# Optimization experiments

Measured on AMD Instinct MI355X. Metric: run time of the kernel, lower is better.

Reference implementation:

```python
import jax, jax.numpy as jnp
import numpy as np

H = 16   # num_heads
G = 4    # groups (code structurally requires 4)
DIM = 1024
HD = DIM // H // G  # 16


def setup_inputs() -> dict:
    key = jax.random.key(0)
    k1, k2, k3 = jax.random.split(key, 3)
    x = jax.random.normal(k1, (8, 4096, DIM), dtype=jnp.float32)
    w_qkvw = jax.random.normal(k2, (DIM, 4 * DIM), dtype=jnp.float32) * 0.02
    w_out = jax.random.normal(k3, (DIM, DIM), dtype=jnp.float32) * 0.02
    return {"x": x, "w_qkvw": w_qkvw, "w_out": w_out}


def reference(x, w_qkvw, w_out):
    B, S, dim = x.shape
    qkvw = x @ w_qkvw  # [B, S, 4*dim]
    # chunk into G groups along last dim -> G tensors of [B, S, dim] (G==4)
    chunks = jnp.split(qkvw, G, axis=-1)
    # each chunk split again into G sub-chunks of [B, S, dim/G]
    subs = [jnp.split(t, G, axis=-1) for t in chunks]
    # torch: q,k,v,w = [cat([qi,ki,vi,wi], dim=0) for qi,ki,vi,wi in zip(*subs)]
    q = jnp.concatenate([subs[i][0] for i in range(4)], axis=0)  # [4B, S, dim/G]
    k = jnp.concatenate([subs[i][1] for i in range(4)], axis=0)
    v = jnp.concatenate([subs[i][2] for i in range(4)], axis=0)
    w = jnp.concatenate([subs[i][3] for i in range(4)], axis=0)
    # faithful row-major reshape: [4B, S, dim/G] -> [4B, H, S, hd] -> transpose(1,2)
    def shp(t):
        return t.reshape(B * G, H, -1, HD).swapaxes(1, 2)  # [4B, S, H, hd]
    q, k, v = shp(q), shp(k), shp(v)
    w = w.reshape(B * G, H, -1, HD)  # [4B, H, S, hd]
    scale = HD ** -0.5
    scores = (q @ k.swapaxes(-2, -1)) * scale          # [4B, S, H, H]
    attn = jax.nn.softmax(scores, axis=-1)
    o = (attn @ v).swapaxes(1, 2).reshape(B, S, dim)   # [B, S, dim]
    return (o * w.reshape(B, S, dim)) @ w_out
```

## Files before the change

kernel.cpp:

```cpp
#include <hip/hip_runtime.h>
#include <hip/hip_bf16.h>
#include <stdint.h>


typedef __bf16 bf16;
typedef __bf16 bf16x8 __attribute__((ext_vector_type(8)));
typedef float f32x4 __attribute__((ext_vector_type(4)));

__device__ __forceinline__ void gload16(const bf16* g, bf16* l) {
  __builtin_amdgcn_global_load_lds(
      (const __attribute__((address_space(1))) void*)g,
      (__attribute__((address_space(3))) void*)l, 16, 0, 0);
}

#define BAR() asm volatile("s_barrier" ::: "memory")
#define SB() __builtin_amdgcn_sched_barrier(0)
#define LGKM0 asm volatile("s_waitcnt lgkmcnt(0)" ::: "memory")
#define PRIO1 __builtin_amdgcn_s_setprio(1)
#define PRIO0 __builtin_amdgcn_s_setprio(0)

#define READ_A(mq, AO)                                                        \
  {                                                                           \
    _Pragma("unroll") for (int i = 0; i < 4; ++i)                             \
        _Pragma("unroll") for (int kk = 0; kk < 2; ++kk)                      \
            a[i][kk] = *(const bf16x8*)(lds + (AO) +                          \
                                        ((mq)*64 + i * 16 + fr) * 128 +       \
                                        ((kk * 64 + fkb) ^ xo));              \
  }
#define READ_B(nh, BO)                                                        \
  {                                                                           \
    _Pragma("unroll") for (int j = 0; j < 2; ++j)                             \
        _Pragma("unroll") for (int kk = 0; kk < 2; ++kk)                      \
            b[(nh)*2 + j][kk] = *(const bf16x8*)(lds + (BO) +                 \
                                                 (bro + (nh)*32 + j * 16 + fr) * 128 + \
                                                 ((kk * 64 + fkb) ^ xo));     \
  }
#define MFMA_Q(mq, nh)                                                        \
  {                                                                           \
    _Pragma("unroll") for (int i = 0; i < 4; ++i)                             \
        _Pragma("unroll") for (int j = 0; j < 2; ++j) {                       \
      acc[(mq)*4 + i][(nh)*2 + j] = __builtin_amdgcn_mfma_f32_16x16x32_bf16(  \
          a[i][0], b[(nh)*2 + j][0], acc[(mq)*4 + i][(nh)*2 + j], 0, 0, 0);   \
      acc[(mq)*4 + i][(nh)*2 + j] = __builtin_amdgcn_mfma_f32_16x16x32_bf16(  \
          a[i][1], b[(nh)*2 + j][1], acc[(mq)*4 + i][(nh)*2 + j], 0, 0, 0);   \
    }                                                                         \
  }
#define STAGE_AH(h, X, base)                                                  \
  {                                                                           \
    const bf16* g = gA + ((h)*128) * 1024 + (X)*64;                           \
    gload16(g, (bf16*)(lds + (base) + (h)*16384 + wv * 1024));                \
    gload16(g + 64 * 1024, (bf16*)(lds + (base) + (h)*16384 + 8192 + wv * 1024)); \
  }
#define STAGE_BH(h, X)                                                        \
  {                                                                           \
    const int ro = 98304 + ((X)&1) * 32768 + (h)*16384;                       \
    const bf16* g = gB + ((h)*128) * 1024 + (X)*64;                           \
    gload16(g, (bf16*)(lds + ro + wv * 1024));                                \
    gload16(g + 64 * 1024, (bf16*)(lds + ro + 8192 + wv * 1024));             \
  }

template <typename OutT>
__global__ __launch_bounds__(512, 2)
void gemm256(const bf16* __restrict__ A, const bf16* __restrict__ BT,
             OutT* __restrict__ C, int N, int super) {
  constexpr int K = 1024;
  __shared__ __align__(16) char smem[163840];
  char* lds = smem;

  const int tid = threadIdx.x;
  const int lane = tid & 63;
  const int wv = tid >> 6;
  const int wr = wv >> 2;
  const int wc = wv & 3;

  const int gx = gridDim.x;
  const int nwg = gx * gridDim.y;
  const int bid = blockIdx.y * gx + blockIdx.x;
  const int xcd = bid & 7;
  const int l = bid >> 3;
  long trow, tcol;
  if (super) {
    const int s = l >> 5, i = l & 31;
    const int colS = gx >> 2;
    trow = xcd * 16 + (s / colS) * 8 + (i >> 2);
    tcol = (s % colS) * 4 + (i & 3);
  } else {
    const int swz = xcd * (nwg >> 3) + l;
    trow = swz / gx;
    tcol = swz % gx;
  }
  const long row0 = trow * 256;
  const long col0 = tcol * 256;

  const int srow = tid >> 3;
  const int scol = (((tid & 7) * 16) ^ ((srow & 7) << 4)) >> 1;
  const bf16* gA = A + (row0 + srow) * K + scol;
  const bf16* gB = BT + (col0 + srow) * K + scol;

  const int fr = lane & 15;
  const int fkb = (lane >> 4) * 16;
  const int xo = (fr & 7) << 4;
  const int bro = (wc & 1) * 64;

  bf16x8 a[4][2], b[4][2];
  f32x4 acc[8][4] = {};

  STAGE_AH(0, 0, 0); STAGE_AH(1, 0, 0);
  STAGE_AH(0, 1, 32768); STAGE_AH(1, 1, 32768);
  STAGE_BH(0, 0); STAGE_BH(1, 0);
  STAGE_BH(0, 1); STAGE_BH(1, 1);
  asm volatile("s_waitcnt vmcnt(4)" ::: "memory");
  SB(); BAR(); SB();
  READ_A(0, wr * 16384);
  READ_B(0, 98304 + (wc >> 1) * 16384);
  SB();

  int ac0 = 0, ac1 = 32768, ac2 = 65536;
  for (int T = 0; T < 16; ++T) {
    const int aoff = ac0 + wr * 16384;
    const int aoffN = ac1 + wr * 16384;
    const int boff = 98304 + (T & 1) * 32768 + (wc >> 1) * 16384;
    const int boffN = 98304 + ((T + 1) & 1) * 32768 + (wc >> 1) * 16384;
    if (T < 14) { STAGE_AH(0, T + 2, ac2); STAGE_AH(1, T + 2, ac2); }
    SB(); BAR(); LGKM0; SB();
    READ_B(1, boff); SB();
    PRIO1; MFMA_Q(0, 0); PRIO0; SB();
    BAR(); LGKM0; SB();
    PRIO1; MFMA_Q(0, 1); PRIO0; SB();
    READ_A(1, aoff); SB();
    BAR(); LGKM0; SB();
    PRIO1; MFMA_Q(1, 1); PRIO0; SB();
    if (T < 14) {
      STAGE_BH(0, T + 2); STAGE_BH(1, T + 2);
      asm volatile("s_waitcnt vmcnt(8)" ::: "memory");
    } else if (T == 14) {
      asm volatile("s_waitcnt vmcnt(0)" ::: "memory");
    }
    SB(); BAR(); LGKM0; SB();
    PRIO1; MFMA_Q(1, 0); PRIO0; SB();
    if (T < 15) { READ_A(0, aoffN); READ_B(0, boffN); }
    SB();
    const int t = ac0; ac0 = ac1; ac1 = ac2; ac2 = t;
  }

  const int crow = (lane >> 4) * 4;
  const int ccol = lane & 15;
  const long rb = row0 + wr * 128;
  const long cb = col0 + wc * 64;
#pragma unroll
  for (int m = 0; m < 8; ++m)
#pragma unroll
    for (int n = 0; n < 4; ++n)
#pragma unroll
      for (int i = 0; i < 4; ++i)
        C[(rb + m * 16 + crow + i) * (long)N + cb + n * 16 + ccol] =
            (OutT)acc[m][n][i];
}

__device__ __forceinline__ void load16f(const bf16* p, float* f) {
  const uint4* u = (const uint4*)p;
  uint4 a = u[0], b = u[1];
  uint32_t w[8] = {a.x, a.y, a.z, a.w, b.x, b.y, b.z, b.w};
#pragma unroll
  for (int j = 0; j < 8; ++j) {
    f[2 * j] = __uint_as_float(w[j] << 16);
    f[2 * j + 1] = __uint_as_float(w[j] & 0xffff0000u);
  }
}

__global__ __launch_bounds__(256)
void attn_fuse(const bf16* __restrict__ qkvw, bf16* __restrict__ ow,
               int b0, long bstride) {
  __shared__ bf16 data[16 * 1024];
  const int s_hi = blockIdx.x;
  const int g = blockIdx.y;
  const int bz = blockIdx.z;
  const int b = b0 + bz;
  const bf16* base = qkvw + (long)bz * bstride;
  const int tid = threadIdx.x;

#pragma unroll
  for (int i = 0; i < 8; ++i) {
    int c = tid + i * 256;
    int h = c >> 7;
    int col = (c & 127) * 8;
    *(uint4*)&data[h * 1024 + col] =
        *(const uint4*)(base + (long)(h * 256 + s_hi) * 4096 + g * 1024 + col);
  }
  __syncthreads();

  const int s_lo = tid >> 4;
  const int h1 = tid & 15;
  const int off = s_lo * 16;

  float q[16], p[16], o[16];
  load16f(&data[h1 * 1024 + off], q);

  float mx = -1e30f;
#pragma unroll
  for (int h2 = 0; h2 < 16; ++h2) {
    float kf[16];
    load16f(&data[h2 * 1024 + 256 + off], kf);
    float s = 0.f;
#pragma unroll
    for (int d = 0; d < 16; ++d) s += q[d] * kf[d];
    s *= 0.25f;
    p[h2] = s;
    mx = fmaxf(mx, s);
  }
  float sum = 0.f;
#pragma unroll
  for (int h2 = 0; h2 < 16; ++h2) {
    float e = __expf(p[h2] - mx);
    p[h2] = e;
    sum += e;
  }
  const float inv = 1.f / sum;
#pragma unroll
  for (int d = 0; d < 16; ++d) o[d] = 0.f;
#pragma unroll
  for (int h2 = 0; h2 < 16; ++h2) {
    float vf[16];
    load16f(&data[h2 * 1024 + 512 + off], vf);
    const float av = p[h2] * inv;
#pragma unroll
    for (int d = 0; d < 16; ++d) o[d] += av * vf[d];
  }
  float wf[16];
  load16f(&data[h1 * 1024 + 768 + off], wf);

  const int bp = g * 8 + b;
  const long R = (long)(bp >> 2) * 4096 + (bp & 3) * 1024 + h1 * 64 + (s_hi >> 2);
  const int cbo = (s_hi & 3) * 256 + off;
  union { uint4 u[2]; bf16 hh[16]; } st;
#pragma unroll
  for (int d = 0; d < 16; ++d) st.hh[d] = (bf16)(o[d] * wf[d]);
  uint4* dst = (uint4*)&ow[R * 1024 + cbo];
  dst[0] = st.u[0];
  dst[1] = st.u[1];
}

__global__ __launch_bounds__(256)
void cast_x_kernel(const float* __restrict__ in, bf16* __restrict__ out, long n4) {
  long i = (long)blockIdx.x * 256 + threadIdx.x;
  if (i >= n4) return;
  float4 v = ((const float4*)in)[i];
  union { uint2 d; bf16 h[4]; } r;
  r.h[0] = (bf16)v.x; r.h[1] = (bf16)v.y; r.h[2] = (bf16)v.z; r.h[3] = (bf16)v.w;
  ((uint2*)out)[i] = r.d;
}

__global__ __launch_bounds__(256)
void tcast_kernel(const float* __restrict__ in, bf16* __restrict__ out, int R, int C) {
  __shared__ float t[64][65];
  const int c0 = blockIdx.x * 64, r0 = blockIdx.y * 64;
  const int lr = threadIdx.x >> 6;
  const int lc = threadIdx.x & 63;
#pragma unroll
  for (int i = 0; i < 16; ++i)
    t[lr + i * 4][lc] = in[(long)(r0 + lr + i * 4) * C + c0 + lc];
  __syncthreads();
#pragma unroll
  for (int i = 0; i < 16; ++i) {
    int oc = lr + i * 4;
    out[(long)(c0 + oc) * R + r0 + lc] = (bf16)t[lc][oc];
  }
}

extern "C" void kernel_launch(void* const* d_in, const int* in_sizes, int n_in,
                              void* d_out, int out_size, void* d_ws, size_t ws_size,
                              hipStream_t stream) {
  const float* x = (const float*)d_in[0];
  const float* w_qkvw = (const float*)d_in[1];
  const float* w_out = (const float*)d_in[2];
  float* out = (float*)d_out;

  char* ws = (char*)d_ws;
  size_t off = 0;
  bf16* x_bf = (bf16*)(ws + off); off += (size_t)32768 * 1024 * 2;
  bf16* bt1  = (bf16*)(ws + off); off += (size_t)4096 * 1024 * 2;
  bf16* bt2  = (bf16*)(ws + off); off += (size_t)1024 * 1024 * 2;
  bf16* owb  = (bf16*)(ws + off); off += (size_t)32768 * 1024 * 2;
  bf16* qk   = (bf16*)(ws + off);
  const size_t rem = ws_size > off ? ws_size - off : 0;
  const size_t full_need = (size_t)32768 * 4096 * 2;

  cast_x_kernel<<<32768, 256, 0, stream>>>(x, x_bf, (long)8388608);
  tcast_kernel<<<dim3(64, 16), 256, 0, stream>>>(w_qkvw, bt1, 1024, 4096);
  tcast_kernel<<<dim3(16, 16), 256, 0, stream>>>(w_out, bt2, 1024, 1024);

  if (rem >= full_need) {
    gemm256<bf16><<<dim3(16, 128), 512, 0, stream>>>(x_bf, bt1, qk, 4096, 1);
    attn_fuse<<<dim3(256, 4, 8), 256, 0, stream>>>(qk, owb, 0, (long)4096 * 4096);
  } else {
    for (int b = 0; b < 8; ++b) {
      gemm256<bf16><<<dim3(16, 16), 512, 0, stream>>>(
          x_bf + (size_t)b * 4096 * 1024, bt1, qk, 4096, 0);
      attn_fuse<<<dim3(256, 4, 1), 256, 0, stream>>>(qk, owb, b, 0);
    }
  }
  gemm256<float><<<dim3(4, 128), 512, 0, stream>>>(owb, bt2, out, 1024, 1);
}
```

Before: 458.3 us.

## Double-buffer A fragments and spread global loads across GEMM main loop phases

```diff
diff --git a/kernel.cpp b/kernel.cpp
--- a/kernel.cpp
+++ b/kernel.cpp
@@ -19,13 +19,13 @@
 #define PRIO1 __builtin_amdgcn_s_setprio(1)
 #define PRIO0 __builtin_amdgcn_s_setprio(0)
 
-#define READ_A(mq, AO)                                                        \
+#define READ_AX(dst, mq, AO)                                                  \
   {                                                                           \
     _Pragma("unroll") for (int i = 0; i < 4; ++i)                             \
         _Pragma("unroll") for (int kk = 0; kk < 2; ++kk)                      \
-            a[i][kk] = *(const bf16x8*)(lds + (AO) +                          \
-                                        ((mq)*64 + i * 16 + fr) * 128 +       \
-                                        ((kk * 64 + fkb) ^ xo));              \
+            dst[i][kk] = *(const bf16x8*)(lds + (AO) +                        \
+                                          ((mq)*64 + i * 16 + fr) * 128 +     \
+                                          ((kk * 64 + fkb) ^ xo));            \
   }
 #define READ_B(nh, BO)                                                        \
   {                                                                           \
@@ -35,14 +35,14 @@
                                                  (bro + (nh)*32 + j * 16 + fr) * 128 + \
                                                  ((kk * 64 + fkb) ^ xo));     \
   }
-#define MFMA_Q(mq, nh)                                                        \
+#define MFMA_Q(arr, mq, nh)                                                   \
   {                                                                           \
     _Pragma("unroll") for (int i = 0; i < 4; ++i)                             \
         _Pragma("unroll") for (int j = 0; j < 2; ++j) {                       \
       acc[(mq)*4 + i][(nh)*2 + j] = __builtin_amdgcn_mfma_f32_16x16x32_bf16(  \
-          a[i][0], b[(nh)*2 + j][0], acc[(mq)*4 + i][(nh)*2 + j], 0, 0, 0);   \
+          arr[i][0], b[(nh)*2 + j][0], acc[(mq)*4 + i][(nh)*2 + j], 0, 0, 0); \
       acc[(mq)*4 + i][(nh)*2 + j] = __builtin_amdgcn_mfma_f32_16x16x32_bf16(  \
-          a[i][1], b[(nh)*2 + j][1], acc[(mq)*4 + i][(nh)*2 + j], 0, 0, 0);   \
+          arr[i][1], b[(nh)*2 + j][1], acc[(mq)*4 + i][(nh)*2 + j], 0, 0, 0); \
     }                                                                         \
   }
 #define STAGE_AH(h, X, base)                                                  \
@@ -102,16 +102,16 @@
   const int xo = (fr & 7) << 4;
   const int bro = (wc & 1) * 64;
 
-  bf16x8 a[4][2], b[4][2];
+  bf16x8 a0[4][2], a1[4][2], b[4][2];
   f32x4 acc[8][4] = {};
 
   STAGE_AH(0, 0, 0); STAGE_AH(1, 0, 0);
+  STAGE_BH(0, 0); STAGE_BH(1, 0);
   STAGE_AH(0, 1, 32768); STAGE_AH(1, 1, 32768);
-  STAGE_BH(0, 0); STAGE_BH(1, 0);
   STAGE_BH(0, 1); STAGE_BH(1, 1);
-  asm volatile("s_waitcnt vmcnt(4)" ::: "memory");
+  asm volatile("s_waitcnt vmcnt(8)" ::: "memory");
   SB(); BAR(); SB();
-  READ_A(0, wr * 16384);
+  READ_AX(a0, 0, wr * 16384);
   READ_B(0, 98304 + (wc >> 1) * 16384);
   SB();
 
@@ -121,24 +121,30 @@
     const int aoffN = ac1 + wr * 16384;
     const int boff = 98304 + (T & 1) * 32768 + (wc >> 1) * 16384;
     const int boffN = 98304 + ((T + 1) & 1) * 32768 + (wc >> 1) * 16384;
-    if (T < 14) { STAGE_AH(0, T + 2, ac2); STAGE_AH(1, T + 2, ac2); }
+    if (T < 14) STAGE_AH(0, T + 2, ac2);
     SB(); BAR(); LGKM0; SB();
     READ_B(1, boff); SB();
-    PRIO1; MFMA_Q(0, 0); PRIO0; SB();
-    BAR(); LGKM0; SB();
-    PRIO1; MFMA_Q(0, 1); PRIO0; SB();
-    READ_A(1, aoff); SB();
-    BAR(); LGKM0; SB();
-    PRIO1; MFMA_Q(1, 1); PRIO0; SB();
+    PRIO1; MFMA_Q(a0, 0, 0); PRIO0; SB();
+    if (T < 14) STAGE_AH(1, T + 2, ac2);
+    SB(); BAR(); LGKM0; SB();
+    PRIO1; MFMA_Q(a0, 0, 1); PRIO0; SB();
+    READ_AX(a1, 1, aoff); SB();
+    BAR();
     if (T < 14) {
-      STAGE_BH(0, T + 2); STAGE_BH(1, T + 2);
-      asm volatile("s_waitcnt vmcnt(8)" ::: "memory");
+      asm volatile("s_waitcnt vmcnt(4)" ::: "memory");
     } else if (T == 14) {
       asm volatile("s_waitcnt vmcnt(0)" ::: "memory");
     }
-    SB(); BAR(); LGKM0; SB();
-    PRIO1; MFMA_Q(1, 0); PRIO0; SB();
-    if (T < 15) { READ_A(0, aoffN); READ_B(0, boffN); }
+    LGKM0; SB();
+    if (T < 14) STAGE_BH(0, T + 2);
+    SB();
+    PRIO1; MFMA_Q(a1, 1, 1); PRIO0; SB();
+    if (T < 15) READ_AX(a0, 0, aoffN);
+    SB();
+    if (T < 14) STAGE_BH(1, T + 2);
+    SB(); BAR(); SB();
+    PRIO1; MFMA_Q(a1, 1, 0); PRIO0; SB();
+    if (T < 15) READ_B(0, boffN);
     SB();
     const int t = ac0; ac0 = ac1; ac1 = ac2; ac2 = t;
   }
```

Measured after the change: 464.7 us. No clear change (+1.4%).
